# Kernel optimization log

Hardware: AMD Instinct MI355X
Metric: run time of the kernel (lower is better)

The kernel has to match this reference:

```python
import jax, jax.numpy as jnp
import numpy as np

NUM_ROUTING = 3
EPS = 1e-8


def squash(s, axis):
    # s * (||s||^2 / (1 + ||s||^2)) / ||s||  along `axis`
    sq = jnp.sum(s * s, axis=axis, keepdims=True)
    return s * (sq / (1.0 + sq)) / jnp.sqrt(sq + EPS)


def setup_inputs() -> dict:
    key = jax.random.key(0)
    k1, k2 = jax.random.split(key)
    B, R, C, OUT, IN = 32, 2048, 32, 32, 16
    x = jax.random.normal(k1, (B, R, IN), dtype=jnp.float32)
    vote = jax.random.normal(k2, (R, C, OUT, IN), dtype=jnp.float32)
    return {"x": x, "vote": vote}


def reference(x, vote):
    # votes[b,r,c,o] = sum_i vote[r,c,o,i] * x[b,r,i]
    votes = jnp.einsum('rcoi,bri->brco', vote, x)  # [B,R,C,OUT]
    agreement = jnp.zeros_like(votes)
    verdict = None
    for _ in range(NUM_ROUTING):
        chairman = jax.nn.softmax(agreement, axis=1)          # softmax over routes
        summary = jnp.sum(chairman * votes, axis=1, keepdims=True)  # [B,1,C,OUT]
        verdict = squash(summary, axis=3)                     # squash over out_dim
        agreement = agreement + jnp.sum(votes * verdict, axis=3, keepdims=True)
    return verdict[:, 0, :, :]  # [B, C, OUT]
```

## Files before the change

kernel.cpp:

```cpp
#include <hip/hip_runtime.h>
#include <hip/hip_fp16.h>

#define B 32
#define R 2048
#define C 32
#define O 32
#define IN 16

typedef _Float16 hf2 __attribute__((ext_vector_type(2)));


__global__ __launch_bounds__(512, 4) void votes_kernel(
    const float* __restrict__ x,
    const float* __restrict__ vote,
    __half* __restrict__ votes_h)
{
  const int t = threadIdx.x;
  const int c = blockIdx.y * 2 + (t >> 8);
  const int tt = t & 255;
  const int rp_l = tt >> 4;
  const int op = tt & 15;
  const int r0 = blockIdx.x * 32;
  const int r = r0 + 2 * rp_l;
  const int rpg = blockIdx.x * 16 + rp_l;

  __shared__ unsigned int x_lds[32 * 32 * 8];

#pragma unroll
  for (int k = 0; k < 8; ++k) {
    int j = t + k * 512;
    int bb = j >> 7;
    int rr = (j >> 2) & 31;
    int ic = j & 3;
    float4 v = *reinterpret_cast<const float4*>(
        x + ((size_t)bb * R + r0 + rr) * IN + ic * 4);
    __half2 h01 = __float22half2_rn(make_float2(v.x, v.y));
    __half2 h23 = __float22half2_rn(make_float2(v.z, v.w));
    int w = (bb * 32 + rr) * 8 + 2 * ic;
    x_lds[w] = __builtin_bit_cast(unsigned int, h01);
    x_lds[w + 1] = __builtin_bit_cast(unsigned int, h23);
  }

  unsigned int wh[4][8];
#pragma unroll
  for (int p = 0; p < 2; ++p) {
#pragma unroll
    for (int q = 0; q < 2; ++q) {
      const float4* vp = reinterpret_cast<const float4*>(
          vote + (((size_t)(r + p) * C + c) * O + 2 * op + q) * IN);
#pragma unroll
      for (int k = 0; k < 4; ++k) {
        float4 f = vp[k];
        __half2 a = __float22half2_rn(make_float2(f.x, f.y));
        __half2 d = __float22half2_rn(make_float2(f.z, f.w));
        wh[p * 2 + q][2 * k] = __builtin_bit_cast(unsigned int, a);
        wh[p * 2 + q][2 * k + 1] = __builtin_bit_cast(unsigned int, d);
      }
    }
  }
  __syncthreads();

  __half* ob = votes_h + (size_t)c * 65536 + (size_t)rpg * 64 + op * 4;

#pragma unroll 2
  for (int bb = 0; bb < 32; ++bb) {
    const uint4* xr = reinterpret_cast<const uint4*>(
        &x_lds[(bb * 32 + 2 * rp_l) * 8]);
    uint4 xa = xr[0], xb = xr[1];
    uint4 xc = xr[2], xd = xr[3];
    unsigned int x0[8] = {xa.x, xa.y, xa.z, xa.w, xb.x, xb.y, xb.z, xb.w};
    unsigned int x1[8] = {xc.x, xc.y, xc.z, xc.w, xd.x, xd.y, xd.z, xd.w};
    float a00 = 0.f, a01 = 0.f, a10 = 0.f, a11 = 0.f;
#pragma unroll
    for (int k = 0; k < 8; ++k) {
      hf2 xv0 = __builtin_bit_cast(hf2, x0[k]);
      hf2 xv1 = __builtin_bit_cast(hf2, x1[k]);
      a00 = __builtin_amdgcn_fdot2(__builtin_bit_cast(hf2, wh[0][k]), xv0, a00, false);
      a01 = __builtin_amdgcn_fdot2(__builtin_bit_cast(hf2, wh[1][k]), xv0, a01, false);
      a10 = __builtin_amdgcn_fdot2(__builtin_bit_cast(hf2, wh[2][k]), xv1, a10, false);
      a11 = __builtin_amdgcn_fdot2(__builtin_bit_cast(hf2, wh[3][k]), xv1, a11, false);
    }
    __half2 w0 = __float22half2_rn(make_float2(a00, a10));
    __half2 w1 = __float22half2_rn(make_float2(a01, a11));
    uint2 pk;
    pk.x = __builtin_bit_cast(unsigned int, w0);
    pk.y = __builtin_bit_cast(unsigned int, w1);
    *reinterpret_cast<uint2*>(ob + (size_t)bb * C * 65536) = pk;
  }
}

#define PIN4(u) asm volatile("" : "+v"(u.x), "+v"(u.y), "+v"(u.z), "+v"(u.w))

__device__ __forceinline__ float rscatter8(const float u[8], int q) {
  const bool h4 = (q & 4) != 0;
  const bool h2 = (q & 2) != 0;
  const bool h1 = (q & 1) != 0;
  float ka = h4 ? u[4] : u[0], sa = h4 ? u[0] : u[4];
  float kb = h4 ? u[5] : u[1], sb = h4 ? u[1] : u[5];
  float kc = h4 ? u[6] : u[2], sc = h4 ? u[2] : u[6];
  float kd = h4 ? u[7] : u[3], sd = h4 ? u[3] : u[7];
  ka += __shfl_xor(sa, 4);
  kb += __shfl_xor(sb, 4);
  kc += __shfl_xor(sc, 4);
  kd += __shfl_xor(sd, 4);
  float pa = h2 ? kc : ka, qa = h2 ? ka : kc;
  float pb = h2 ? kd : kb, qb = h2 ? kb : kd;
  pa += __shfl_xor(qa, 2);
  pb += __shfl_xor(qb, 2);
  float ra = h1 ? pb : pa, rs = h1 ? pa : pb;
  ra += __shfl_xor(rs, 1);
  return ra;
}

__global__ __launch_bounds__(1024, 4) void routing_kernel(
    const __half* __restrict__ votes_h,
    float* __restrict__ out)
{
  const int b = blockIdx.x >> 5;
  const int c = blockIdx.x & 31;
  const int t = threadIdx.x;
  const int lane = t & 63;
  const int wave = t >> 6;
  const int q = t & 7;
  const int rb = t >> 3;

  __shared__ float2 e2s[1032];
  __shared__ float4 red4[16][8];
  __shared__ float vdf[32];
  __shared__ float scal_z[16];

  const uint4* src = reinterpret_cast<const uint4*>(
      votes_h + ((size_t)b * C + c) * 65536);
  uint4 v[8];
#pragma unroll
  for (int k = 0; k < 8; ++k) v[k] = src[t + k * 1024];
#pragma unroll
  for (int k = 0; k < 8; ++k) PIN4(v[k]);

  float a0 = 0.f, a1 = 0.f;
  const hf2 ones = {(_Float16)1.0f, (_Float16)1.0f};

#pragma unroll
  for (int iter = 0; iter < 3; ++iter) {
    if (iter > 0) {
      float e0 = __expf(a0), e1 = __expf(a1);
      float z = e0 + e1;
#pragma unroll
      for (int mask = 32; mask; mask >>= 1) z += __shfl_xor(z, mask);
      if (lane == 0) scal_z[wave] = z;
      e2s[rb + 129 * q] = make_float2(e0, e1);
      __syncthreads();
    }

    float s0 = 0.f, s1 = 0.f, s2 = 0.f, s3 = 0.f;
    if (iter == 0) {
#pragma unroll
      for (int k = 0; k < 8; ++k) {
        s0 = __builtin_amdgcn_fdot2(__builtin_bit_cast(hf2, v[k].x), ones, s0, false);
        s1 = __builtin_amdgcn_fdot2(__builtin_bit_cast(hf2, v[k].y), ones, s1, false);
        s2 = __builtin_amdgcn_fdot2(__builtin_bit_cast(hf2, v[k].z), ones, s2, false);
        s3 = __builtin_amdgcn_fdot2(__builtin_bit_cast(hf2, v[k].w), ones, s3, false);
      }
    } else {
#pragma unroll
      for (int k = 0; k < 8; ++k) {
        float2 e = e2s[rb + 129 * k];
        __half2 h0 = __builtin_bit_cast(__half2, v[k].x);
        __half2 h1 = __builtin_bit_cast(__half2, v[k].y);
        __half2 h2 = __builtin_bit_cast(__half2, v[k].z);
        __half2 h3 = __builtin_bit_cast(__half2, v[k].w);
        s0 += e.x * __low2float(h0) + e.y * __high2float(h0);
        s1 += e.x * __low2float(h1) + e.y * __high2float(h1);
        s2 += e.x * __low2float(h2) + e.y * __high2float(h2);
        s3 += e.x * __low2float(h3) + e.y * __high2float(h3);
      }
    }
    s0 += __shfl_xor(s0, 8);  s1 += __shfl_xor(s1, 8);
    s2 += __shfl_xor(s2, 8);  s3 += __shfl_xor(s3, 8);
    s0 += __shfl_xor(s0, 16); s1 += __shfl_xor(s1, 16);
    s2 += __shfl_xor(s2, 16); s3 += __shfl_xor(s3, 16);
    s0 += __shfl_xor(s0, 32); s1 += __shfl_xor(s1, 32);
    s2 += __shfl_xor(s2, 32); s3 += __shfl_xor(s3, 32);
    if (lane < 8) red4[wave][lane] = make_float4(s0, s1, s2, s3);
    __syncthreads();

    if (t < 32) {
      const float* redf = reinterpret_cast<const float*>(red4);
      float S = 0.f;
#pragma unroll
      for (int w = 0; w < 16; ++w) S += redf[w * 32 + t];
      float Zinv;
      if (iter == 0) {
        Zinv = 1.0f / 2048.0f;
      } else {
        float Z = 0.f;
#pragma unroll
        for (int w = 0; w < 16; ++w) Z += scal_z[w];
        Zinv = 1.0f / Z;
      }
      float summary = S * Zinv;
      float sq = summary * summary;
#pragma unroll
      for (int mask = 16; mask; mask >>= 1) sq += __shfl_xor(sq, mask);
      float scale = sq / ((1.0f + sq) * sqrtf(sq + 1e-8f));
      float vd = summary * scale;
      if (iter < 2) vdf[t] = vd;
      else out[((size_t)b * C + c) * O + t] = vd;
    }

    if (iter < 2) {
      __syncthreads();
      float4 vd4 = *reinterpret_cast<const float4*>(&vdf[4 * q]);
      float u[8];
#pragma unroll
      for (int k = 0; k < 8; ++k) {
        __half2 h0 = __builtin_bit_cast(__half2, v[k].x);
        __half2 h1 = __builtin_bit_cast(__half2, v[k].y);
        __half2 h2 = __builtin_bit_cast(__half2, v[k].z);
        __half2 h3 = __builtin_bit_cast(__half2, v[k].w);
        u[k] = __low2float(h0) * vd4.x + __low2float(h1) * vd4.y +
               __low2float(h2) * vd4.z + __low2float(h3) * vd4.w;
      }
      a0 += rscatter8(u, q);
#pragma unroll
      for (int k = 0; k < 8; ++k) {
        __half2 h0 = __builtin_bit_cast(__half2, v[k].x);
        __half2 h1 = __builtin_bit_cast(__half2, v[k].y);
        __half2 h2 = __builtin_bit_cast(__half2, v[k].z);
        __half2 h3 = __builtin_bit_cast(__half2, v[k].w);
        u[k] = __high2float(h0) * vd4.x + __high2float(h1) * vd4.y +
               __high2float(h2) * vd4.z + __high2float(h3) * vd4.w;
      }
      a1 += rscatter8(u, q);
    }
  }
}

extern "C" void kernel_launch(void* const* d_in, const int* in_sizes, int n_in,
                              void* d_out, int out_size, void* d_ws, size_t ws_size,
                              hipStream_t stream) {
  const float* x = (const float*)d_in[0];
  const float* vote = (const float*)d_in[1];
  float* out = (float*)d_out;
  __half* votes_h = (__half*)d_ws;

  votes_kernel<<<dim3(R / 32, C / 2), 512, 0, stream>>>(x, vote, votes_h);
  routing_kernel<<<dim3(B * C), 1024, 0, stream>>>(votes_h, out);
}
```

Baseline: 275.6 us.

## Process two route tiles per votes block with register prefetch of next weights

Each votes_kernel block now handles two consecutive 32-route tiles, which halves the grid. While the current tile is computed, the next tile's vote weights are prefetched into registers, overlapping their global loads with the fdot2 loop. This costs 64 extra float registers per thread for the prefetch buffer plus an extra barrier per tile, which may lower occupancy under launch_bounds(512,4) and reduces the number of blocks available for parallelism.

```diff
diff --git a/kernel.cpp b/kernel.cpp
--- a/kernel.cpp
+++ b/kernel.cpp
@@ -6,6 +6,7 @@
 #define C 32
 #define O 32
 #define IN 16
+#define NT 2
 
 typedef _Float16 hf2 __attribute__((ext_vector_type(2)));
 
@@ -20,72 +21,101 @@
   const int tt = t & 255;
   const int rp_l = tt >> 4;
   const int op = tt & 15;
-  const int r0 = blockIdx.x * 32;
-  const int r = r0 + 2 * rp_l;
-  const int rpg = blockIdx.x * 16 + rp_l;
+  const int rbase = blockIdx.x * (32 * NT);
 
   __shared__ unsigned int x_lds[32 * 32 * 8];
 
-#pragma unroll
-  for (int k = 0; k < 8; ++k) {
-    int j = t + k * 512;
-    int bb = j >> 7;
-    int rr = (j >> 2) & 31;
-    int ic = j & 3;
-    float4 v = *reinterpret_cast<const float4*>(
-        x + ((size_t)bb * R + r0 + rr) * IN + ic * 4);
-    __half2 h01 = __float22half2_rn(make_float2(v.x, v.y));
-    __half2 h23 = __float22half2_rn(make_float2(v.z, v.w));
-    int w = (bb * 32 + rr) * 8 + 2 * ic;
-    x_lds[w] = __builtin_bit_cast(unsigned int, h01);
-    x_lds[w + 1] = __builtin_bit_cast(unsigned int, h23);
+  float4 nf[16];
+  {
+    const int r = rbase + 2 * rp_l;
+#pragma unroll
+    for (int p = 0; p < 2; ++p) {
+#pragma unroll
+      for (int q = 0; q < 2; ++q) {
+        const float4* vp = reinterpret_cast<const float4*>(
+            vote + (((size_t)(r + p) * C + c) * O + 2 * op + q) * IN);
+#pragma unroll
+        for (int k = 0; k < 4; ++k) nf[(p * 2 + q) * 4 + k] = vp[k];
+      }
+    }
   }
 
-  unsigned int wh[4][8];
-#pragma unroll
-  for (int p = 0; p < 2; ++p) {
-#pragma unroll
-    for (int q = 0; q < 2; ++q) {
-      const float4* vp = reinterpret_cast<const float4*>(
-          vote + (((size_t)(r + p) * C + c) * O + 2 * op + q) * IN);
+#pragma unroll
+  for (int tile = 0; tile < NT; ++tile) {
+    const int r0 = rbase + tile * 32;
+    const int rpg = (rbase >> 1) + tile * 16 + rp_l;
+
+#pragma unroll
+    for (int k = 0; k < 8; ++k) {
+      int j = t + k * 512;
+      int bb = j >> 7;
+      int rr = (j >> 2) & 31;
+      int ic = j & 3;
+      float4 v = *reinterpret_cast<const float4*>(
+          x + ((size_t)bb * R + r0 + rr) * IN + ic * 4);
+      __half2 h01 = __float22half2_rn(make_float2(v.x, v.y));
+      __half2 h23 = __float22half2_rn(make_float2(v.z, v.w));
+      int w = (bb * 32 + rr) * 8 + 2 * ic;
+      x_lds[w] = __builtin_bit_cast(unsigned int, h01);
+      x_lds[w + 1] = __builtin_bit_cast(unsigned int, h23);
+    }
+    __syncthreads();
+
+    unsigned int wh[4][8];
+#pragma unroll
+    for (int f = 0; f < 4; ++f) {
 #pragma unroll
       for (int k = 0; k < 4; ++k) {
-        float4 f = vp[k];
-        __half2 a = __float22half2_rn(make_float2(f.x, f.y));
-        __half2 d = __float22half2_rn(make_float2(f.z, f.w));
-        wh[p * 2 + q][2 * k] = __builtin_bit_cast(unsigned int, a);
-        wh[p * 2 + q][2 * k + 1] = __builtin_bit_cast(unsigned int, d);
-      }
-    }
-  }
-  __syncthreads();
-
-  __half* ob = votes_h + (size_t)c * 65536 + (size_t)rpg * 64 + op * 4;
+        float4 fv = nf[f * 4 + k];
+        __half2 a = __float22half2_rn(make_float2(fv.x, fv.y));
+        __half2 d = __float22half2_rn(make_float2(fv.z, fv.w));
+        wh[f][2 * k] = __builtin_bit_cast(unsigned int, a);
+        wh[f][2 * k + 1] = __builtin_bit_cast(unsigned int, d);
+      }
+    }
+
+    if (tile + 1 < NT) {
+      const int r = rbase + (tile + 1) * 32 + 2 * rp_l;
+#pragma unroll
+      for (int p = 0; p < 2; ++p) {
+#pragma unroll
+        for (int q = 0; q < 2; ++q) {
+          const float4* vp = reinterpret_cast<const float4*>(
+              vote + (((size_t)(r + p) * C + c) * O + 2 * op + q) * IN);
+#pragma unroll
+          for (int k = 0; k < 4; ++k) nf[(p * 2 + q) * 4 + k] = vp[k];
+        }
+      }
+    }
+
+    __half* ob = votes_h + (size_t)c * 65536 + (size_t)rpg * 64 + op * 4;
 
 #pragma unroll 2
-  for (int bb = 0; bb < 32; ++bb) {
-    const uint4* xr = reinterpret_cast<const uint4*>(
-        &x_lds[(bb * 32 + 2 * rp_l) * 8]);
-    uint4 xa = xr[0], xb = xr[1];
-    uint4 xc = xr[2], xd = xr[3];
-    unsigned int x0[8] = {xa.x, xa.y, xa.z, xa.w, xb.x, xb.y, xb.z, xb.w};
-    unsigned int x1[8] = {xc.x, xc.y, xc.z, xc.w, xd.x, xd.y, xd.z, xd.w};
-    float a00 = 0.f, a01 = 0.f, a10 = 0.f, a11 = 0.f;
-#pragma unroll
-    for (int k = 0; k < 8; ++k) {
-      hf2 xv0 = __builtin_bit_cast(hf2, x0[k]);
-      hf2 xv1 = __builtin_bit_cast(hf2, x1[k]);
-      a00 = __builtin_amdgcn_fdot2(__builtin_bit_cast(hf2, wh[0][k]), xv0, a00, false);
-      a01 = __builtin_amdgcn_fdot2(__builtin_bit_cast(hf2, wh[1][k]), xv0, a01, false);
-      a10 = __builtin_amdgcn_fdot2(__builtin_bit_cast(hf2, wh[2][k]), xv1, a10, false);
-      a11 = __builtin_amdgcn_fdot2(__builtin_bit_cast(hf2, wh[3][k]), xv1, a11, false);
-    }
-    __half2 w0 = __float22half2_rn(make_float2(a00, a10));
-    __half2 w1 = __float22half2_rn(make_float2(a01, a11));
-    uint2 pk;
-    pk.x = __builtin_bit_cast(unsigned int, w0);
-    pk.y = __builtin_bit_cast(unsigned int, w1);
-    *reinterpret_cast<uint2*>(ob + (size_t)bb * C * 65536) = pk;
+    for (int bb = 0; bb < 32; ++bb) {
+      const uint4* xr = reinterpret_cast<const uint4*>(
+          &x_lds[(bb * 32 + 2 * rp_l) * 8]);
+      uint4 xa = xr[0], xb = xr[1];
+      uint4 xc = xr[2], xd = xr[3];
+      unsigned int x0[8] = {xa.x, xa.y, xa.z, xa.w, xb.x, xb.y, xb.z, xb.w};
+      unsigned int x1[8] = {xc.x, xc.y, xc.z, xc.w, xd.x, xd.y, xd.z, xd.w};
+      float a00 = 0.f, a01 = 0.f, a10 = 0.f, a11 = 0.f;
+#pragma unroll
+      for (int k = 0; k < 8; ++k) {
+        hf2 xv0 = __builtin_bit_cast(hf2, x0[k]);
+        hf2 xv1 = __builtin_bit_cast(hf2, x1[k]);
+        a00 = __builtin_amdgcn_fdot2(__builtin_bit_cast(hf2, wh[0][k]), xv0, a00, false);
+        a01 = __builtin_amdgcn_fdot2(__builtin_bit_cast(hf2, wh[1][k]), xv0, a01, false);
+        a10 = __builtin_amdgcn_fdot2(__builtin_bit_cast(hf2, wh[2][k]), xv1, a10, false);
+        a11 = __builtin_amdgcn_fdot2(__builtin_bit_cast(hf2, wh[3][k]), xv1, a11, false);
+      }
+      __half2 w0 = __float22half2_rn(make_float2(a00, a10));
+      __half2 w1 = __float22half2_rn(make_float2(a01, a11));
+      uint2 pk;
+      pk.x = __builtin_bit_cast(unsigned int, w0);
+      pk.y = __builtin_bit_cast(unsigned int, w1);
+      *reinterpret_cast<uint2*>(ob + (size_t)bb * C * 65536) = pk;
+    }
+    __syncthreads();
   }
 }
 
@@ -244,6 +274,6 @@
   float* out = (float*)d_out;
   __half* votes_h = (__half*)d_ws;
 
-  votes_kernel<<<dim3(R / 32, C / 2), 512, 0, stream>>>(x, vote, votes_h);
+  votes_kernel<<<dim3(R / (32 * NT), C / 2), 512, 0, stream>>>(x, vote, votes_h);
   routing_kernel<<<dim3(B * C), 1024, 0, stream>>>(votes_h, out);
 }
```

New measurement: 295.0 us. 1.07x slower.
